# Kernel tuning notes

Hardware: AMD Instinct MI355X
Metric: run time of the kernel (lower is better)

## Reference

```python
import jax, jax.numpy as jnp
import numpy as np

B, D_IN, RANK, UNITS = 8192, 4096, 2048, 4096

def setup_inputs() -> dict:
    key = jax.random.key(0)
    k1, k2, k3, k4 = jax.random.split(key, 4)
    inputs = jax.random.normal(k1, (B, D_IN), dtype=jnp.float32)
    U = jax.random.normal(k2, (D_IN, RANK), dtype=jnp.float32) / np.sqrt(D_IN)
    S = jax.random.uniform(k3, (RANK,), dtype=jnp.float32)
    V = jax.random.normal(k4, (UNITS, RANK), dtype=jnp.float32) / np.sqrt(UNITS)
    bias = jnp.zeros((UNITS,), dtype=jnp.float32)
    return {"inputs": inputs, "U": U, "S": S, "V": V, "bias": bias}

def reference(inputs, U, S, V, bias):
    # kernel = U @ diag(S) @ V^T; out = relu(inputs @ kernel + bias)
    # Computed in factored form (same math, avoids dense [D_IN, UNITS] kernel):
    h = (inputs @ U) * S            # [B, rank]
    out = h @ V.T + bias            # [B, units]
    return jax.nn.relu(out)
```

## Files before the change

### kernel.cpp

```cpp
#include <hip/hip_runtime.h>
#include <hip/hip_bf16.h>

#define BSZ   8192
#define DIN   4096
#define RNK   2048
#define UNT   4096

typedef __attribute__((ext_vector_type(4))) float  f32x4;
typedef __attribute__((ext_vector_type(8))) float  f32x8;
typedef __attribute__((ext_vector_type(8))) short  s16x8;
typedef __attribute__((ext_vector_type(8))) unsigned short u16x8;

typedef unsigned short u16;

__device__ __forceinline__ u16 f2bf(float f) {
    unsigned int u = __builtin_bit_cast(unsigned int, f);
    return (u16)((u + 0x7fffu + ((u >> 16) & 1u)) >> 16);
}

__global__ void cvt_bf16_kernel(const float* __restrict__ x,
                                u16* __restrict__ y, int n8) {
    int i = blockIdx.x * blockDim.x + threadIdx.x;
    if (i >= n8) return;
    f32x8 v = ((const f32x8*)x)[i];
    u16x8 o;
#pragma unroll
    for (int j = 0; j < 8; ++j) o[j] = f2bf(v[j]);
    ((u16x8*)y)[i] = o;
}

__global__ void transpose_scale_kernel(const float* __restrict__ U,
                                       const float* __restrict__ S,
                                       u16* __restrict__ Ut) {
    __shared__ float tile[32][33];
    const int r0 = blockIdx.x * 32;
    const int k0 = blockIdx.y * 32;
    const int tx = threadIdx.x;
    const int ty = threadIdx.y;
#pragma unroll
    for (int i = 0; i < 32; i += 8)
        tile[ty + i][tx] = U[(size_t)(k0 + ty + i) * RNK + r0 + tx];
    __syncthreads();
#pragma unroll
    for (int i = 0; i < 32; i += 8) {
        int r = r0 + ty + i;
        Ut[(size_t)r * DIN + k0 + tx] = f2bf(tile[tx][ty + i] * S[r]);
    }
}

__device__ __forceinline__ void glds16(const void* g, void* l) {
    __builtin_amdgcn_global_load_lds(
        (const __attribute__((address_space(1))) unsigned int*)g,
        (__attribute__((address_space(3))) unsigned int*)l,
        16, 0, 0);
}

template <int K, bool RELU_BIAS>
__global__ __launch_bounds__(512) void gemm256(
    const u16* __restrict__ A, const u16* __restrict__ Bt,
    void* __restrict__ C, const float* __restrict__ bias, int N) {
    __shared__ u16 As[2][256 * 64];
    __shared__ u16 Bs[2][256 * 64];

    const int t = threadIdx.x;

    const int gx = gridDim.x;
    const int nwg = gx * gridDim.y;
    int bid = blockIdx.y * gx + blockIdx.x;
    bid = (bid & 7) * (nwg >> 3) + (bid >> 3);
    const int rowBase = (bid / gx) * 256;
    const int colBase = (bid % gx) * 256;

    const int sRow = t >> 3;
    const int sCol = ((t & 7) ^ (sRow & 7)) << 3;
    const u16* aS = A  + (size_t)(rowBase + sRow) * K + sCol;
    const u16* bS = Bt + (size_t)(colBase + sRow) * K + sCol;

#define STG(SRC, DST, h_, Tk_, b_) do {                                       \
    const u16* s_ = (SRC) + (size_t)(h_) * 128 * K + (size_t)(Tk_) * 64;      \
    glds16(s_,                  &DST[b_][(h_) * 8192 + t * 8]);               \
    glds16(s_ + (size_t)64 * K, &DST[b_][(h_) * 8192 + 4096 + t * 8]);        \
} while (0)

    const int lane = t & 63;
    const int wave = t >> 6;
    const int wm = wave >> 2;
    const int wn = wave & 3;
    const int lr = lane & 15;
    const int lg = lane >> 4;
    const int r7 = lr & 7;
    const int swz0 = ((lg    ) ^ r7) << 4;
    const int swz1 = ((lg + 4) ^ r7) << 4;
    const int aRowB = (wm * 128 + lr) * 128;
    const int bRowB = (wn * 64  + lr) * 128;

    f32x4 acc[8][4] = {};
    s16x8 af[8][2], bf[2][2];

    STG(aS, As, 0, 0, 0); STG(aS, As, 1, 0, 0);
    STG(bS, Bs, 0, 0, 0); STG(bS, Bs, 1, 0, 0);
    STG(aS, As, 0, 1, 1); STG(aS, As, 1, 1, 1);
    asm volatile("s_waitcnt vmcnt(4)" ::: "memory");
    __builtin_amdgcn_s_barrier();

    const int NT = K / 64;
    for (int T = 0; T < NT; ++T) {
        const int cur = T & 1, nxt = cur ^ 1;
        const char* aP = (const char*)&As[cur][0] + aRowB;
        const char* bP = (const char*)&Bs[cur][0] + bRowB;

#pragma unroll
        for (int mi = 0; mi < 4; ++mi) {
            af[mi][0] = *(const s16x8*)(aP + mi * 2048 + swz0);
            af[mi][1] = *(const s16x8*)(aP + mi * 2048 + swz1);
        }
#pragma unroll
        for (int nj = 0; nj < 2; ++nj) {
            bf[nj][0] = *(const s16x8*)(bP + nj * 2048 + swz0);
            bf[nj][1] = *(const s16x8*)(bP + nj * 2048 + swz1);
        }
        if (T + 1 < NT) STG(bS, Bs, 0, T + 1, nxt);
        asm volatile("" ::: "memory");
        __builtin_amdgcn_s_barrier();
        asm volatile("s_waitcnt lgkmcnt(0)" ::: "memory");
        __builtin_amdgcn_sched_barrier(0);
        __builtin_amdgcn_s_setprio(1);
#pragma unroll
        for (int mi = 0; mi < 4; ++mi)
#pragma unroll
            for (int nj = 0; nj < 2; ++nj)
#pragma unroll
                for (int kk = 0; kk < 2; ++kk)
                    acc[mi][nj] = __builtin_amdgcn_mfma_f32_16x16x32_bf16(
                        af[mi][kk], bf[nj][kk], acc[mi][nj], 0, 0, 0);
        __builtin_amdgcn_s_setprio(0);
        asm volatile("" ::: "memory");
        __builtin_amdgcn_s_barrier();

#pragma unroll
        for (int mi = 0; mi < 4; ++mi) {
            af[4 + mi][0] = *(const s16x8*)(aP + (4 + mi) * 2048 + swz0);
            af[4 + mi][1] = *(const s16x8*)(aP + (4 + mi) * 2048 + swz1);
        }
        if (T + 1 < NT) STG(bS, Bs, 1, T + 1, nxt);
        asm volatile("" ::: "memory");
        __builtin_amdgcn_s_barrier();
        asm volatile("s_waitcnt lgkmcnt(0)" ::: "memory");
        __builtin_amdgcn_sched_barrier(0);
        __builtin_amdgcn_s_setprio(1);
#pragma unroll
        for (int mi = 0; mi < 4; ++mi)
#pragma unroll
            for (int nj = 0; nj < 2; ++nj)
#pragma unroll
                for (int kk = 0; kk < 2; ++kk)
                    acc[4 + mi][nj] = __builtin_amdgcn_mfma_f32_16x16x32_bf16(
                        af[4 + mi][kk], bf[nj][kk], acc[4 + mi][nj], 0, 0, 0);
        __builtin_amdgcn_s_setprio(0);
        asm volatile("" ::: "memory");
        __builtin_amdgcn_s_barrier();

#pragma unroll
        for (int nj = 0; nj < 2; ++nj) {
            bf[nj][0] = *(const s16x8*)(bP + (2 + nj) * 2048 + swz0);
            bf[nj][1] = *(const s16x8*)(bP + (2 + nj) * 2048 + swz1);
        }
        if (T + 2 < NT) STG(aS, As, 0, T + 2, cur);
        asm volatile("" ::: "memory");
        __builtin_amdgcn_s_barrier();
        asm volatile("s_waitcnt lgkmcnt(0)" ::: "memory");
        __builtin_amdgcn_sched_barrier(0);
        __builtin_amdgcn_s_setprio(1);
#pragma unroll
        for (int mi = 0; mi < 4; ++mi)
#pragma unroll
            for (int nj = 0; nj < 2; ++nj)
#pragma unroll
                for (int kk = 0; kk < 2; ++kk)
                    acc[mi][2 + nj] = __builtin_amdgcn_mfma_f32_16x16x32_bf16(
                        af[mi][kk], bf[nj][kk], acc[mi][2 + nj], 0, 0, 0);
        __builtin_amdgcn_s_setprio(0);
        asm volatile("" ::: "memory");
        __builtin_amdgcn_s_barrier();

        if (T + 2 < NT) STG(aS, As, 1, T + 2, cur);
        asm volatile("" ::: "memory");
        __builtin_amdgcn_s_barrier();
        __builtin_amdgcn_s_setprio(1);
#pragma unroll
        for (int mi = 0; mi < 4; ++mi)
#pragma unroll
            for (int nj = 0; nj < 2; ++nj)
#pragma unroll
                for (int kk = 0; kk < 2; ++kk)
                    acc[4 + mi][2 + nj] = __builtin_amdgcn_mfma_f32_16x16x32_bf16(
                        af[4 + mi][kk], bf[nj][kk], acc[4 + mi][2 + nj], 0, 0, 0);
        __builtin_amdgcn_s_setprio(0);
        if (T + 2 < NT) {
            asm volatile("s_waitcnt vmcnt(4)" ::: "memory");
        } else if (T + 1 < NT) {
            asm volatile("s_waitcnt vmcnt(0)" ::: "memory");
        }
        asm volatile("" ::: "memory");
        __builtin_amdgcn_s_barrier();
    }
#undef STG

    const int cRow = rowBase + wm * 128 + lg * 4;
    const int cCol = colBase + wn * 64 + lr;
    if (RELU_BIAS) {
        float* Cf = (float*)C;
#pragma unroll
        for (int n = 0; n < 4; ++n) {
            const int col = cCol + n * 16;
            const float bv = bias[col];
#pragma unroll
            for (int m = 0; m < 8; ++m) {
#pragma unroll
                for (int r = 0; r < 4; ++r) {
                    float v = acc[m][n][r] + bv;
                    Cf[(size_t)(cRow + m * 16 + r) * N + col] = v > 0.f ? v : 0.f;
                }
            }
        }
    } else {
        u16* Cb = (u16*)C;
#pragma unroll
        for (int n = 0; n < 4; ++n) {
            const int col = cCol + n * 16;
#pragma unroll
            for (int m = 0; m < 8; ++m) {
#pragma unroll
                for (int r = 0; r < 4; ++r)
                    Cb[(size_t)(cRow + m * 16 + r) * N + col] = f2bf(acc[m][n][r]);
            }
        }
    }
}

extern "C" void kernel_launch(void* const* d_in, const int* in_sizes, int n_in,
                              void* d_out, int out_size, void* d_ws, size_t ws_size,
                              hipStream_t stream) {
    const float* X    = (const float*)d_in[0];
    const float* U    = (const float*)d_in[1];
    const float* S    = (const float*)d_in[2];
    const float* V    = (const float*)d_in[3];
    const float* bias = (const float*)d_in[4];
    float* out = (float*)d_out;

    char* ws = (char*)d_ws;
    u16* Xb  = (u16*)ws;
    u16* Utb = (u16*)(ws + ((size_t)64 << 20));
    u16* Vb  = (u16*)(ws + ((size_t)80 << 20));
    u16* Hb  = (u16*)(ws + ((size_t)96 << 20));

    {
        int n8 = (BSZ * DIN) / 8;
        cvt_bf16_kernel<<<n8 / 256, 256, 0, stream>>>(X, Xb, n8);
    }
    {
        dim3 grid(RNK / 32, DIN / 32), block(32, 8);
        transpose_scale_kernel<<<grid, block, 0, stream>>>(U, S, Utb);
    }
    {
        int n8 = (UNT * RNK) / 8;
        cvt_bf16_kernel<<<n8 / 256, 256, 0, stream>>>(V, Vb, n8);
    }
    {
        dim3 grid(RNK / 256, BSZ / 256);
        gemm256<DIN, false><<<grid, 512, 0, stream>>>(Xb, Utb, Hb, nullptr, RNK);
    }
    {
        dim3 grid(UNT / 256, BSZ / 256);
        gemm256<RNK, true><<<grid, 512, 0, stream>>>(Hb, Vb, out, bias, UNT);
    }
}
```

Measured before the change: 576.9 us.

## Collapse four-phase GEMM main loop into two phases with fewer barriers

```diff
diff --git a/kernel.cpp b/kernel.cpp
--- a/kernel.cpp
+++ b/kernel.cpp
@@ -54,6 +54,8 @@
         (__attribute__((address_space(3))) unsigned int*)l,
         16, 0, 0);
 }
+
+#define LDS_FENCE() asm volatile("" ::: "memory")
 
 template <int K, bool RELU_BIAS>
 __global__ __launch_bounds__(512) void gemm256(
@@ -101,7 +103,9 @@
     STG(bS, Bs, 0, 0, 0); STG(bS, Bs, 1, 0, 0);
     STG(aS, As, 0, 1, 1); STG(aS, As, 1, 1, 1);
     asm volatile("s_waitcnt vmcnt(4)" ::: "memory");
+    LDS_FENCE();
     __builtin_amdgcn_s_barrier();
+    LDS_FENCE();
 
     const int NT = K / 64;
     for (int T = 0; T < NT; ++T) {
@@ -109,8 +113,9 @@
         const char* aP = (const char*)&As[cur][0] + aRowB;
         const char* bP = (const char*)&Bs[cur][0] + bRowB;
 
-#pragma unroll
-        for (int mi = 0; mi < 4; ++mi) {
+        if (T + 1 < NT) { STG(bS, Bs, 0, T + 1, nxt); STG(bS, Bs, 1, T + 1, nxt); }
+#pragma unroll
+        for (int mi = 0; mi < 8; ++mi) {
             af[mi][0] = *(const s16x8*)(aP + mi * 2048 + swz0);
             af[mi][1] = *(const s16x8*)(aP + mi * 2048 + swz1);
         }
@@ -119,90 +124,44 @@
             bf[nj][0] = *(const s16x8*)(bP + nj * 2048 + swz0);
             bf[nj][1] = *(const s16x8*)(bP + nj * 2048 + swz1);
         }
-        if (T + 1 < NT) STG(bS, Bs, 0, T + 1, nxt);
-        asm volatile("" ::: "memory");
-        __builtin_amdgcn_s_barrier();
-        asm volatile("s_waitcnt lgkmcnt(0)" ::: "memory");
-        __builtin_amdgcn_sched_barrier(0);
         __builtin_amdgcn_s_setprio(1);
 #pragma unroll
-        for (int mi = 0; mi < 4; ++mi)
-#pragma unroll
-            for (int nj = 0; nj < 2; ++nj)
-#pragma unroll
-                for (int kk = 0; kk < 2; ++kk)
+        for (int kk = 0; kk < 2; ++kk)
+#pragma unroll
+            for (int mi = 0; mi < 8; ++mi)
+#pragma unroll
+                for (int nj = 0; nj < 2; ++nj)
                     acc[mi][nj] = __builtin_amdgcn_mfma_f32_16x16x32_bf16(
                         af[mi][kk], bf[nj][kk], acc[mi][nj], 0, 0, 0);
         __builtin_amdgcn_s_setprio(0);
-        asm volatile("" ::: "memory");
+        LDS_FENCE();
         __builtin_amdgcn_s_barrier();
-
-#pragma unroll
-        for (int mi = 0; mi < 4; ++mi) {
-            af[4 + mi][0] = *(const s16x8*)(aP + (4 + mi) * 2048 + swz0);
-            af[4 + mi][1] = *(const s16x8*)(aP + (4 + mi) * 2048 + swz1);
-        }
-        if (T + 1 < NT) STG(bS, Bs, 1, T + 1, nxt);
-        asm volatile("" ::: "memory");
-        __builtin_amdgcn_s_barrier();
-        asm volatile("s_waitcnt lgkmcnt(0)" ::: "memory");
-        __builtin_amdgcn_sched_barrier(0);
-        __builtin_amdgcn_s_setprio(1);
-#pragma unroll
-        for (int mi = 0; mi < 4; ++mi)
-#pragma unroll
-            for (int nj = 0; nj < 2; ++nj)
-#pragma unroll
-                for (int kk = 0; kk < 2; ++kk)
-                    acc[4 + mi][nj] = __builtin_amdgcn_mfma_f32_16x16x32_bf16(
-                        af[4 + mi][kk], bf[nj][kk], acc[4 + mi][nj], 0, 0, 0);
-        __builtin_amdgcn_s_setprio(0);
-        asm volatile("" ::: "memory");
-        __builtin_amdgcn_s_barrier();
-
+        LDS_FENCE();
+
+        if (T + 2 < NT) { STG(aS, As, 0, T + 2, cur); STG(aS, As, 1, T + 2, cur); }
 #pragma unroll
         for (int nj = 0; nj < 2; ++nj) {
             bf[nj][0] = *(const s16x8*)(bP + (2 + nj) * 2048 + swz0);
             bf[nj][1] = *(const s16x8*)(bP + (2 + nj) * 2048 + swz1);
         }
-        if (T + 2 < NT) STG(aS, As, 0, T + 2, cur);
-        asm volatile("" ::: "memory");
-        __builtin_amdgcn_s_barrier();
-        asm volatile("s_waitcnt lgkmcnt(0)" ::: "memory");
-        __builtin_amdgcn_sched_barrier(0);
         __builtin_amdgcn_s_setprio(1);
 #pragma unroll
-        for (int mi = 0; mi < 4; ++mi)
-#pragma unroll
-            for (int nj = 0; nj < 2; ++nj)
-#pragma unroll
-                for (int kk = 0; kk < 2; ++kk)
+        for (int kk = 0; kk < 2; ++kk)
+#pragma unroll
+            for (int mi = 0; mi < 8; ++mi)
+#pragma unroll
+                for (int nj = 0; nj < 2; ++nj)
                     acc[mi][2 + nj] = __builtin_amdgcn_mfma_f32_16x16x32_bf16(
                         af[mi][kk], bf[nj][kk], acc[mi][2 + nj], 0, 0, 0);
-        __builtin_amdgcn_s_setprio(0);
-        asm volatile("" ::: "memory");
-        __builtin_amdgcn_s_barrier();
-
-        if (T + 2 < NT) STG(aS, As, 1, T + 2, cur);
-        asm volatile("" ::: "memory");
-        __builtin_amdgcn_s_barrier();
-        __builtin_amdgcn_s_setprio(1);
-#pragma unroll
-        for (int mi = 0; mi < 4; ++mi)
-#pragma unroll
-            for (int nj = 0; nj < 2; ++nj)
-#pragma unroll
-                for (int kk = 0; kk < 2; ++kk)
-                    acc[4 + mi][2 + nj] = __builtin_amdgcn_mfma_f32_16x16x32_bf16(
-                        af[4 + mi][kk], bf[nj][kk], acc[4 + mi][2 + nj], 0, 0, 0);
         __builtin_amdgcn_s_setprio(0);
         if (T + 2 < NT) {
             asm volatile("s_waitcnt vmcnt(4)" ::: "memory");
         } else if (T + 1 < NT) {
             asm volatile("s_waitcnt vmcnt(0)" ::: "memory");
         }
-        asm volatile("" ::: "memory");
+        LDS_FENCE();
         __builtin_amdgcn_s_barrier();
+        LDS_FENCE();
     }
 #undef STG
 
```

After: 539.0 us. -6.6%, faster.
